# Kernel optimization log

Measured on AMD Instinct MI355X. Metric: run time of the kernel, lower is better.

## Reference

```python
import jax, jax.numpy as jnp
import numpy as np

N_NODES = 50000
N_EDGES = 640000
IN_CH = 128
HIDDEN = 128
HEADS = 4
HEAD_DIM = HIDDEN // HEADS  # 32
NEG_SLOPE = 0.2


def setup_inputs() -> dict:
    key = jax.random.key(0)
    ks = jax.random.split(key, 12)
    x = jax.random.normal(ks[0], (N_NODES, IN_CH), dtype=jnp.float32)
    edge_index = jax.random.randint(ks[1], (2, N_EDGES), 0, N_NODES, dtype=jnp.int64)
    s = 0.1
    W1 = jax.random.normal(ks[2], (IN_CH, HEADS * HEAD_DIM), dtype=jnp.float32) * s
    a_src1 = jax.random.normal(ks[3], (HEADS, HEAD_DIM), dtype=jnp.float32) * s
    a_dst1 = jax.random.normal(ks[4], (HEADS, HEAD_DIM), dtype=jnp.float32) * s
    b1 = jax.random.normal(ks[5], (HEADS * HEAD_DIM,), dtype=jnp.float32) * s
    W2 = jax.random.normal(ks[6], (HIDDEN, HEADS * HEAD_DIM), dtype=jnp.float32) * s
    a_src2 = jax.random.normal(ks[7], (HEADS, HEAD_DIM), dtype=jnp.float32) * s
    a_dst2 = jax.random.normal(ks[8], (HEADS, HEAD_DIM), dtype=jnp.float32) * s
    b2 = jax.random.normal(ks[9], (HEADS * HEAD_DIM,), dtype=jnp.float32) * s
    return {"x": x, "edge_index": edge_index, "W1": W1, "a_src1": a_src1,
            "a_dst1": a_dst1, "b1": b1, "W2": W2, "a_src2": a_src2,
            "a_dst2": a_dst2, "b2": b2}


def _gat_conv(x, src, dst, W, a_src, a_dst, b):
    """PyG GATConv (concat=True, add_self_loops already applied to src/dst)."""
    N = x.shape[0]
    H, C = a_src.shape
    h = (x @ W).reshape(N, H, C)                      # [N, H, C]
    alpha_s = jnp.einsum('nhc,hc->nh', h, a_src)      # [N, H]
    alpha_d = jnp.einsum('nhc,hc->nh', h, a_dst)      # [N, H]
    e = alpha_s[src] + alpha_d[dst]                   # [E, H]
    e = jnp.where(e > 0, e, NEG_SLOPE * e)            # leaky_relu(0.2)
    # segment softmax over destination nodes (every node has a self-loop)
    emax = jax.ops.segment_max(e, dst, num_segments=N)
    ee = jnp.exp(e - emax[dst])
    denom = jax.ops.segment_sum(ee, dst, num_segments=N)
    alpha = ee / (denom[dst] + 1e-16)                 # [E, H]
    out = jax.ops.segment_sum(h[src] * alpha[:, :, None], dst, num_segments=N)
    return out.reshape(N, H * C) + b


def reference(x, edge_index, W1, a_src1, a_dst1, b1, W2, a_src2, a_dst2, b2):
    N = x.shape[0]
    loops = jnp.arange(N, dtype=edge_index.dtype)
    src = jnp.concatenate([edge_index[0], loops])
    dst = jnp.concatenate([edge_index[1], loops])
    h = _gat_conv(x, src, dst, W1, a_src1, a_dst1, b1)
    h = jax.nn.relu(h)  # dropout is identity in eval mode
    out = _gat_conv(h, src, dst, W2, a_src2, a_dst2, b2)
    return out
```

## Files before the change

### kernel.cpp

```cpp
#include <hip/hip_runtime.h>
#include <hip/hip_bf16.h>
#include <hip/hip_fp16.h>

#define N_NODES 50000
#define N_EDGES 640000
#define E_TOT   690000
#define CH      128
#define ROWPAD  50176
#define GEMMB   391
#define EBLK    2048
#define NEB     337
#define NBUCK   196
#define CAP     4608

typedef __attribute__((ext_vector_type(8))) short short8;
typedef __attribute__((ext_vector_type(4))) float float4v;

static __device__ __forceinline__ float bf2f(unsigned short u) {
  return __uint_as_float(((unsigned)u) << 16);
}
static __device__ __forceinline__ unsigned short f2bf(float f) {
  unsigned u = __float_as_uint(f);
  return (unsigned short)((u + 0x7fffu + ((u >> 16) & 1u)) >> 16);
}

static __device__ __forceinline__ void load_edge(const int* __restrict__ ei,
                                                 int e, int i64, int& s, int& d)
{
  if (e >= N_EDGES) { s = d = e - N_EDGES; return; }
  if (i64) { s = ei[2 * (size_t)e]; d = ei[2 * ((size_t)N_EDGES + e)]; }
  else     { s = ei[e];             d = ei[N_EDGES + e]; }
}

static __device__ __forceinline__ short8 load_bf8(const void* __restrict__ X,
                                                  size_t off, int f32)
{
  if (!f32) return *(const short8*)((const unsigned short*)X + off);
  const float4* p = (const float4*)((const float*)X + off);
  float4 u = p[0], v = p[1];
  short8 r;
  r[0] = (short)f2bf(u.x); r[1] = (short)f2bf(u.y);
  r[2] = (short)f2bf(u.z); r[3] = (short)f2bf(u.w);
  r[4] = (short)f2bf(v.x); r[5] = (short)f2bf(v.y);
  r[6] = (short)f2bf(v.z); r[7] = (short)f2bf(v.w);
  return r;
}

__global__ __launch_bounds__(256) void k_prep(
    const void* __restrict__ W1, const void* __restrict__ W2,
    const void* __restrict__ as1, const void* __restrict__ ad1,
    const void* __restrict__ as2, const void* __restrict__ ad2,
    unsigned short* __restrict__ Wt1, unsigned short* __restrict__ Wt2,
    unsigned short* __restrict__ Ba1, unsigned short* __restrict__ Ba2,
    const unsigned short* __restrict__ x16,
    const unsigned int* __restrict__ eiw,
    int* __restrict__ flags, int* __restrict__ gcur)
{
  int b = blockIdx.x, t = threadIdx.x;
  __shared__ int sf, si;
  if (t == 0) { sf = 0; si = 1; }
  __syncthreads();
  int bad = 0;
  for (int i = t; i < 4096; i += 256) {
    float v = bf2f(x16[i]);
    if (!(v == v) || fabsf(v) > 100.f) bad = 1;
  }
  if (bad) atomicOr(&sf, 1);
  if (b == 0 && t < 128 && eiw[2 * t + 1] != 0u) atomicAnd(&si, 0);
  __syncthreads();
  int f32 = sf;
  if (b == 0 && t == 0) { flags[0] = sf; flags[1] = si; }
  if (b == 0 && t < NBUCK) gcur[t] = t * CAP;

  if (b < 8) {
    int g = b * 256 + t;
    int l = g >> 10;
    int rem = g & 1023;
    int k = rem >> 3, n = rem & 7;
    const void* W  = l ? W2 : W1;
    const void* av = (n < 4) ? (l ? as2 : as1) : (l ? ad2 : ad1);
    int h = n & 3;
    float sum = 0.f;
    for (int c = 0; c < 32; c++) {
      float w = f32 ? ((const float*)W)[k * 128 + h * 32 + c]
                    : bf2f(((const unsigned short*)W)[k * 128 + h * 32 + c]);
      float a = f32 ? ((const float*)av)[h * 32 + c]
                    : bf2f(((const unsigned short*)av)[h * 32 + c]);
      sum += w * a;
    }
    unsigned short* Ba = l ? Ba2 : Ba1;
    Ba[n * 128 + k] = f2bf(sum);
    Ba[(8 + (rem >> 7)) * 128 + (rem & 127)] = 0;
  } else {
    int b2 = b - 8;
    int l = b2 >> 7, c = b2 & 127;
    if (t < 128) {
      const void* W = l ? W2 : W1;
      unsigned short* Wt = l ? Wt2 : Wt1;
      Wt[c * 128 + t] = f32 ? f2bf(((const float*)W)[t * 128 + c])
                            : ((const unsigned short*)W)[t * 128 + c];
    }
  }
}

struct SmemG { unsigned short WB[144][136]; };

static __device__ __forceinline__ void gemm_body(
    SmemG& sm, int bx,
    const void* __restrict__ X,
    const unsigned short* __restrict__ Wt_g,
    const unsigned short* __restrict__ Ba_g,
    unsigned short* __restrict__ H, float* __restrict__ AS,
    float* __restrict__ AD, int nrows, int xf32)
{
  int tid = threadIdx.x;
#pragma unroll
  for (int i = 0; i < 8; i++) {
    int j = i * 256 + tid;
    int c = j >> 4, k8 = j & 15;
    *(short8*)&sm.WB[c][k8 * 8] = *(const short8*)(Wt_g + c * 128 + k8 * 8);
  }
  {
    int n = tid >> 4, k8 = tid & 15;
    *(short8*)&sm.WB[128 + n][k8 * 8] = *(const short8*)(Ba_g + n * 128 + k8 * 8);
  }
  __syncthreads();
  int wave = tid >> 6, lane = tid & 63;
  int R0 = (bx * 4 + wave) * 32;
  if (R0 >= nrows) return;
  int m = lane & 15, quad = lane >> 4;
  int rA = R0 + m;        if (rA >= nrows) rA = nrows - 1;
  int rB = R0 + 16 + m;   if (rB >= nrows) rB = nrows - 1;
  size_t aA = (size_t)rA * CH + quad * 8;
  size_t aB = (size_t)rB * CH + quad * 8;
  float4v acc[2][8];
  float4v accA[2];
#pragma unroll
  for (int hf = 0; hf < 2; hf++) {
    accA[hf] = (float4v){0.f, 0.f, 0.f, 0.f};
#pragma unroll
    for (int ct = 0; ct < 8; ct++) acc[hf][ct] = (float4v){0.f, 0.f, 0.f, 0.f};
  }
#pragma unroll
  for (int kb = 0; kb < 4; kb++) {
    short8 a0 = load_bf8(X, aA + kb * 32, xf32);
    short8 a1 = load_bf8(X, aB + kb * 32, xf32);
#pragma unroll
    for (int ct = 0; ct < 8; ct++) {
      short8 bb = *(const short8*)&sm.WB[ct * 16 + m][kb * 32 + quad * 8];
      acc[0][ct] = __builtin_amdgcn_mfma_f32_16x16x32_bf16(a0, bb, acc[0][ct], 0, 0, 0);
      acc[1][ct] = __builtin_amdgcn_mfma_f32_16x16x32_bf16(a1, bb, acc[1][ct], 0, 0, 0);
    }
    short8 bA = *(const short8*)&sm.WB[128 + m][kb * 32 + quad * 8];
    accA[0] = __builtin_amdgcn_mfma_f32_16x16x32_bf16(a0, bA, accA[0], 0, 0, 0);
    accA[1] = __builtin_amdgcn_mfma_f32_16x16x32_bf16(a1, bA, accA[1], 0, 0, 0);
  }
#pragma unroll
  for (int hf = 0; hf < 2; hf++) {
    int rbase = R0 + hf * 16 + quad * 4;
#pragma unroll
    for (int ct = 0; ct < 8; ct++) {
      int col = ct * 16 + m;
#pragma unroll
      for (int r = 0; r < 4; r++)
        H[(size_t)(rbase + r) * CH + col] = __half_as_ushort(__float2half(acc[hf][ct][r]));
    }
    if (m < 4) {
#pragma unroll
      for (int r = 0; r < 4; r++)
        AS[(size_t)(rbase + r) * 4 + m] = accA[hf][r];
    } else if (m < 8) {
#pragma unroll
      for (int r = 0; r < 4; r++)
        AD[(size_t)(rbase + r) * 4 + (m - 4)] = accA[hf][r];
    }
  }
}

__global__ __launch_bounds__(256, 2) void k_gemm(
    const void* __restrict__ X,
    const unsigned short* __restrict__ Wt_g,
    const unsigned short* __restrict__ Ba_g,
    unsigned short* __restrict__ H, float* __restrict__ AS, float* __restrict__ AD,
    int nrows)
{
  __shared__ SmemG sm;
  gemm_body(sm, blockIdx.x, X, Wt_g, Ba_g, H, AS, AD, nrows, 0);
}

__global__ __launch_bounds__(256, 2) void k_gemm_scat(
    const void* __restrict__ X,
    const unsigned short* __restrict__ Wt_g,
    const unsigned short* __restrict__ Ba_g,
    unsigned short* __restrict__ H, float* __restrict__ AS, float* __restrict__ AD,
    int nrows, const int* __restrict__ ei, int* __restrict__ gcur,
    unsigned int* __restrict__ ebuf, const int* __restrict__ flags)
{
  __shared__ SmemG sm;
  __shared__ int hist[NBUCK];
  __shared__ int cur[NBUCK];
  if (blockIdx.x >= GEMMB) {
    int b = blockIdx.x - GEMMB;
    int t = threadIdx.x;
    if (t < NBUCK) hist[t] = 0;
    __syncthreads();
    int i64 = flags[1];
    int base = b * EBLK;
    int sA[8], dA[8];
#pragma unroll
    for (int k = 0; k < 8; k++) {
      int e = base + k * 256 + t;
      sA[k] = -1;
      if (e < E_TOT) {
        load_edge(ei, e, i64, sA[k], dA[k]);
        atomicAdd(&hist[dA[k] >> 8], 1);
      }
    }
    __syncthreads();
    if (t < NBUCK) {
      int c = hist[t];
      cur[t] = c ? atomicAdd(&gcur[t], c) : 0;
    }
    __syncthreads();
#pragma unroll
    for (int k = 0; k < 8; k++) {
      if (sA[k] >= 0) {
        int pos = atomicAdd(&cur[dA[k] >> 8], 1);
        ebuf[pos] = ((unsigned)sA[k] << 8) | (unsigned)(dA[k] & 255);
      }
    }
    return;
  }
  gemm_body(sm, blockIdx.x, X, Wt_g, Ba_g, H, AS, AD, nrows, flags[0]);
}

__global__ __launch_bounds__(256) void k_fine(
    const unsigned int* __restrict__ ebuf, const int* __restrict__ gcur,
    int2* __restrict__ rpdeg, unsigned short* __restrict__ csr)
{
  __shared__ int cnt[256], sh[256], cur[256];
  int q = blockIdx.x, t = threadIdx.x;
  int lo = q * CAP, hi = gcur[q];
  cnt[t] = 0;
  __syncthreads();
  for (int i = lo + t; i < hi; i += 256)
    atomicAdd(&cnt[ebuf[i] & 255u], 1);
  __syncthreads();
  int v = cnt[t];
  sh[t] = v;
  __syncthreads();
  for (int off = 1; off < 256; off <<= 1) {
    int u = (t >= off) ? sh[t - off] : 0;
    __syncthreads();
    sh[t] += u;
    __syncthreads();
  }
  int lp = sh[t] - v;
  int n = (q << 8) + t;
  if (n < N_NODES) rpdeg[n] = make_int2(lo + lp, v);
  cur[t] = lo + lp;
  __syncthreads();
  for (int i = lo + t; i < hi; i += 256) {
    unsigned p = ebuf[i];
    int slot = atomicAdd(&cur[p & 255u], 1);
    csr[slot] = (unsigned short)(p >> 8);
  }
}

__global__ __launch_bounds__(256) void k_agg(
    const int2* __restrict__ rpdeg,
    const unsigned short* __restrict__ csr,
    const __half* __restrict__ H,
    const float* __restrict__ AS, const float* __restrict__ AD,
    const void* __restrict__ b, void* __restrict__ Y,
    const int* __restrict__ flags, int layer)
{
  int tid = threadIdx.x;
  int node = blockIdx.x * 4 + (tid >> 6);
  if (node >= N_NODES) return;
  int lane = tid & 63;
  int h = lane >> 4;
  int c0 = 2 * lane;
  int2 rd = rpdeg[node];
  int start = rd.x, dg = rd.y;
  float adh = AD[(size_t)node * 4 + h];
  const __half2* __restrict__ H2 = (const __half2*)H;
  float accx = 0.f, accy = 0.f, den = 0.f;
  int last = start + dg - 1;
  for (int j = 0; j < dg; j += 16) {
    int sI[16];
#pragma unroll
    for (int u = 0; u < 16; u++) {
      int idx = start + j + u;
      sI[u] = (int)csr[idx <= last ? idx : last];
    }
    float2 vV[16];
#pragma unroll
    for (int u = 0; u < 16; u++)
      vV[u] = __half22float2(H2[sI[u] * 64 + lane]);
    float eV[16];
#pragma unroll
    for (int u = 0; u < 16; u++)
      eV[u] = AS[sI[u] * 4 + h] + adh;
#pragma unroll
    for (int u = 0; u < 16; u++) {
      float x = eV[u] > 0.f ? eV[u] : 0.2f * eV[u];
      float ex = (j + u < dg) ? __expf(x) : 0.f;
      accx += ex * vV[u].x;
      accy += ex * vV[u].y;
      den  += ex;
    }
  }
  float inv = 1.f / (den + 1e-16f);
  int f32 = flags[0];
  float b0 = f32 ? ((const float*)b)[c0]     : bf2f(((const unsigned short*)b)[c0]);
  float b1 = f32 ? ((const float*)b)[c0 + 1] : bf2f(((const unsigned short*)b)[c0 + 1]);
  float r0 = accx * inv + b0;
  float r1 = accy * inv + b1;
  size_t o = (size_t)node * CH + c0;
  if (layer == 1) {
    r0 = r0 > 0.f ? r0 : 0.f;
    r1 = r1 > 0.f ? r1 : 0.f;
    ushort2 w; w.x = f2bf(r0); w.y = f2bf(r1);
    *(ushort2*)((unsigned short*)Y + o) = w;
  } else if (f32) {
    float2 w; w.x = r0; w.y = r1;
    *(float2*)((float*)Y + o) = w;
  } else {
    ushort2 w; w.x = f2bf(r0); w.y = f2bf(r1);
    *(ushort2*)((unsigned short*)Y + o) = w;
  }
}

extern "C" void kernel_launch(void* const* d_in, const int* in_sizes, int n_in,
                              void* d_out, int out_size, void* d_ws, size_t ws_size,
                              hipStream_t stream)
{
  const void* x   = d_in[0];
  const int*  ei  = (const int*)d_in[1];
  const void* W1  = d_in[2];
  const void* as1 = d_in[3];
  const void* ad1 = d_in[4];
  const void* b1  = d_in[5];
  const void* W2  = d_in[6];
  const void* as2 = d_in[7];
  const void* ad2 = d_in[8];
  const void* b2  = d_in[9];

  char* ws = (char*)d_ws;
  unsigned short* H   = (unsigned short*)(ws);
  float*  AS          = (float*)(ws + 12845056);
  float*  AD          = (float*)(ws + 13647872);
  unsigned short* X2  = (unsigned short*)(ws + 14450688);
  int2*   rpdeg       = (int2*)(ws + 27295744);
  unsigned short* csr = (unsigned short*)(ws + 27695744);
  unsigned int* ebuf  = (unsigned int*)(ws + 29502080);
  int*    gcur        = (int*)(ws + 33114752);
  int*    flags       = (int*)(ws + 33115648);
  unsigned short* Wt1 = (unsigned short*)(ws + 33116672);
  unsigned short* Wt2 = (unsigned short*)(ws + 33149440);
  unsigned short* Ba1 = (unsigned short*)(ws + 33182208);
  unsigned short* Ba2 = (unsigned short*)(ws + 33186304);

  const int agg_blocks = (N_NODES + 3) / 4;

  k_prep<<<264, 256, 0, stream>>>(W1, W2, as1, ad1, as2, ad2,
                                  Wt1, Wt2, Ba1, Ba2,
                                  (const unsigned short*)x,
                                  (const unsigned int*)ei, flags, gcur);

  k_gemm_scat<<<GEMMB + NEB, 256, 0, stream>>>(
      x, Wt1, Ba1, H, AS, AD, N_NODES, ei, gcur, ebuf, flags);

  k_fine<<<NBUCK, 256, 0, stream>>>(ebuf, gcur, rpdeg, csr);

  k_agg<<<agg_blocks, 256, 0, stream>>>(rpdeg, csr,
                                        (const __half*)H, AS, AD,
                                        b1, X2, flags, 1);

  k_gemm<<<GEMMB, 256, 0, stream>>>(X2, Wt2, Ba2, H, AS, AD, N_NODES);
  k_agg<<<agg_blocks, 256, 0, stream>>>(rpdeg, csr,
                                        (const __half*)H, AS, AD,
                                        b2, d_out, flags, 2);
}
```

Measured before the change: 212.2 us.

## Fuse layer-1 aggregation with layer-2 GEMM through shared memory

Adds a kernel in which each block aggregates 128 nodes for layer 1 (softmax-weighted gather, bias, ReLU). It writes the bf16 results into shared memory and then runs the layer-2 MFMA projection and attention-logit GEMM on that tile. This removes the global X2 round trip and one kernel launch, and layer 2 now writes to separate H/AS/AD buffers. The trade-off is parallelism: the fused kernel uses only 391 blocks, and each wave walks 32 nodes in sequence. That leaves far fewer waves in flight to hide gather latency than the previous 12500-block aggregation kernel had.

```diff
diff --git a/kernel.cpp b/kernel.cpp
--- a/kernel.cpp
+++ b/kernel.cpp
@@ -105,6 +105,23 @@
 
 struct SmemG { unsigned short WB[144][136]; };
 
+static __device__ __forceinline__ void stage_wb(
+    SmemG& sm, const unsigned short* __restrict__ Wt_g,
+    const unsigned short* __restrict__ Ba_g)
+{
+  int tid = threadIdx.x;
+#pragma unroll
+  for (int i = 0; i < 8; i++) {
+    int j = i * 256 + tid;
+    int c = j >> 4, k8 = j & 15;
+    *(short8*)&sm.WB[c][k8 * 8] = *(const short8*)(Wt_g + c * 128 + k8 * 8);
+  }
+  {
+    int n = tid >> 4, k8 = tid & 15;
+    *(short8*)&sm.WB[128 + n][k8 * 8] = *(const short8*)(Ba_g + n * 128 + k8 * 8);
+  }
+}
+
 static __device__ __forceinline__ void gemm_body(
     SmemG& sm, int bx,
     const void* __restrict__ X,
@@ -114,16 +131,7 @@
     float* __restrict__ AD, int nrows, int xf32)
 {
   int tid = threadIdx.x;
-#pragma unroll
-  for (int i = 0; i < 8; i++) {
-    int j = i * 256 + tid;
-    int c = j >> 4, k8 = j & 15;
-    *(short8*)&sm.WB[c][k8 * 8] = *(const short8*)(Wt_g + c * 128 + k8 * 8);
-  }
-  {
-    int n = tid >> 4, k8 = tid & 15;
-    *(short8*)&sm.WB[128 + n][k8 * 8] = *(const short8*)(Ba_g + n * 128 + k8 * 8);
-  }
+  stage_wb(sm, Wt_g, Ba_g);
   __syncthreads();
   int wave = tid >> 6, lane = tid & 63;
   int R0 = (bx * 4 + wave) * 32;
@@ -175,17 +183,6 @@
         AD[(size_t)(rbase + r) * 4 + (m - 4)] = accA[hf][r];
     }
   }
-}
-
-__global__ __launch_bounds__(256, 2) void k_gemm(
-    const void* __restrict__ X,
-    const unsigned short* __restrict__ Wt_g,
-    const unsigned short* __restrict__ Ba_g,
-    unsigned short* __restrict__ H, float* __restrict__ AS, float* __restrict__ AD,
-    int nrows)
-{
-  __shared__ SmemG sm;
-  gemm_body(sm, blockIdx.x, X, Wt_g, Ba_g, H, AS, AD, nrows, 0);
 }
 
 __global__ __launch_bounds__(256, 2) void k_gemm_scat(
@@ -267,13 +264,139 @@
   }
 }
 
+static __device__ __forceinline__ void agg_node(
+    const unsigned short* __restrict__ csr,
+    const __half2* __restrict__ H2,
+    const float* __restrict__ AS, float adh,
+    int start, int dg, int lane, int h,
+    float& accx, float& accy, float& den)
+{
+  int last = start + dg - 1;
+  for (int j = 0; j < dg; j += 16) {
+    int sI[16];
+#pragma unroll
+    for (int u = 0; u < 16; u++) {
+      int idx = start + j + u;
+      sI[u] = (int)csr[idx <= last ? idx : last];
+    }
+    float2 vV[16];
+#pragma unroll
+    for (int u = 0; u < 16; u++)
+      vV[u] = __half22float2(H2[sI[u] * 64 + lane]);
+    float eV[16];
+#pragma unroll
+    for (int u = 0; u < 16; u++)
+      eV[u] = AS[sI[u] * 4 + h] + adh;
+#pragma unroll
+    for (int u = 0; u < 16; u++) {
+      float x = eV[u] > 0.f ? eV[u] : 0.2f * eV[u];
+      float ex = (j + u < dg) ? __expf(x) : 0.f;
+      accx += ex * vV[u].x;
+      accy += ex * vV[u].y;
+      den  += ex;
+    }
+  }
+}
+
+struct SmemF { unsigned short WB[144][136]; unsigned short X2t[128][136]; };
+
+__global__ __launch_bounds__(256, 2) void k_agg_gemm(
+    const int2* __restrict__ rpdeg,
+    const unsigned short* __restrict__ csr,
+    const __half* __restrict__ H_in,
+    const float* __restrict__ AS_in, const float* __restrict__ AD_in,
+    const void* __restrict__ b1,
+    const unsigned short* __restrict__ Wt_g,
+    const unsigned short* __restrict__ Ba_g,
+    unsigned short* __restrict__ H, float* __restrict__ AS, float* __restrict__ AD,
+    const int* __restrict__ flags)
+{
+  __shared__ SmemF sm;
+  int tid = threadIdx.x;
+  stage_wb(*(SmemG*)&sm, Wt_g, Ba_g);
+
+  int wave = tid >> 6, lane = tid & 63;
+  int h = lane >> 4;
+  int c0 = 2 * lane;
+  int f32 = flags[0];
+  const __half2* __restrict__ H2 = (const __half2*)H_in;
+  float b0 = f32 ? ((const float*)b1)[c0]     : bf2f(((const unsigned short*)b1)[c0]);
+  float bb1 = f32 ? ((const float*)b1)[c0 + 1] : bf2f(((const unsigned short*)b1)[c0 + 1]);
+
+  for (int i = 0; i < 32; i++) {
+    int loc = wave * 32 + i;
+    int node = blockIdx.x * 128 + loc;
+    float r0 = 0.f, r1 = 0.f;
+    if (node < N_NODES) {
+      int2 rd = rpdeg[node];
+      float adh = AD_in[(size_t)node * 4 + h];
+      float accx = 0.f, accy = 0.f, den = 0.f;
+      agg_node(csr, H2, AS_in, adh, rd.x, rd.y, lane, h, accx, accy, den);
+      float inv = 1.f / (den + 1e-16f);
+      r0 = accx * inv + b0;
+      r1 = accy * inv + bb1;
+      r0 = r0 > 0.f ? r0 : 0.f;
+      r1 = r1 > 0.f ? r1 : 0.f;
+    }
+    sm.X2t[loc][c0]     = f2bf(r0);
+    sm.X2t[loc][c0 + 1] = f2bf(r1);
+  }
+  __syncthreads();
+
+  int m = lane & 15, quad = lane >> 4;
+  int R0l = wave * 32;
+  float4v acc[2][8];
+  float4v accA[2];
+#pragma unroll
+  for (int hf = 0; hf < 2; hf++) {
+    accA[hf] = (float4v){0.f, 0.f, 0.f, 0.f};
+#pragma unroll
+    for (int ct = 0; ct < 8; ct++) acc[hf][ct] = (float4v){0.f, 0.f, 0.f, 0.f};
+  }
+#pragma unroll
+  for (int kb = 0; kb < 4; kb++) {
+    short8 a0 = *(const short8*)&sm.X2t[R0l + m][kb * 32 + quad * 8];
+    short8 a1 = *(const short8*)&sm.X2t[R0l + 16 + m][kb * 32 + quad * 8];
+#pragma unroll
+    for (int ct = 0; ct < 8; ct++) {
+      short8 bb = *(const short8*)&sm.WB[ct * 16 + m][kb * 32 + quad * 8];
+      acc[0][ct] = __builtin_amdgcn_mfma_f32_16x16x32_bf16(a0, bb, acc[0][ct], 0, 0, 0);
+      acc[1][ct] = __builtin_amdgcn_mfma_f32_16x16x32_bf16(a1, bb, acc[1][ct], 0, 0, 0);
+    }
+    short8 bA = *(const short8*)&sm.WB[128 + m][kb * 32 + quad * 8];
+    accA[0] = __builtin_amdgcn_mfma_f32_16x16x32_bf16(a0, bA, accA[0], 0, 0, 0);
+    accA[1] = __builtin_amdgcn_mfma_f32_16x16x32_bf16(a1, bA, accA[1], 0, 0, 0);
+  }
+  int Rg = blockIdx.x * 128 + R0l;
+#pragma unroll
+  for (int hf = 0; hf < 2; hf++) {
+    int rbase = Rg + hf * 16 + quad * 4;
+#pragma unroll
+    for (int ct = 0; ct < 8; ct++) {
+      int col = ct * 16 + m;
+#pragma unroll
+      for (int r = 0; r < 4; r++)
+        H[(size_t)(rbase + r) * CH + col] = __half_as_ushort(__float2half(acc[hf][ct][r]));
+    }
+    if (m < 4) {
+#pragma unroll
+      for (int r = 0; r < 4; r++)
+        AS[(size_t)(rbase + r) * 4 + m] = accA[hf][r];
+    } else if (m < 8) {
+#pragma unroll
+      for (int r = 0; r < 4; r++)
+        AD[(size_t)(rbase + r) * 4 + (m - 4)] = accA[hf][r];
+    }
+  }
+}
+
 __global__ __launch_bounds__(256) void k_agg(
     const int2* __restrict__ rpdeg,
     const unsigned short* __restrict__ csr,
     const __half* __restrict__ H,
     const float* __restrict__ AS, const float* __restrict__ AD,
     const void* __restrict__ b, void* __restrict__ Y,
-    const int* __restrict__ flags, int layer)
+    const int* __restrict__ flags)
 {
   int tid = threadIdx.x;
   int node = blockIdx.x * 4 + (tid >> 6);
@@ -282,35 +405,10 @@
   int h = lane >> 4;
   int c0 = 2 * lane;
   int2 rd = rpdeg[node];
-  int start = rd.x, dg = rd.y;
   float adh = AD[(size_t)node * 4 + h];
   const __half2* __restrict__ H2 = (const __half2*)H;
   float accx = 0.f, accy = 0.f, den = 0.f;
-  int last = start + dg - 1;
-  for (int j = 0; j < dg; j += 16) {
-    int sI[16];
-#pragma unroll
-    for (int u = 0; u < 16; u++) {
-      int idx = start + j + u;
-      sI[u] = (int)csr[idx <= last ? idx : last];
-    }
-    float2 vV[16];
-#pragma unroll
-    for (int u = 0; u < 16; u++)
-      vV[u] = __half22float2(H2[sI[u] * 64 + lane]);
-    float eV[16];
-#pragma unroll
-    for (int u = 0; u < 16; u++)
-      eV[u] = AS[sI[u] * 4 + h] + adh;
-#pragma unroll
-    for (int u = 0; u < 16; u++) {
-      float x = eV[u] > 0.f ? eV[u] : 0.2f * eV[u];
-      float ex = (j + u < dg) ? __expf(x) : 0.f;
-      accx += ex * vV[u].x;
-      accy += ex * vV[u].y;
-      den  += ex;
-    }
-  }
+  agg_node(csr, H2, AS, adh, rd.x, rd.y, lane, h, accx, accy, den);
   float inv = 1.f / (den + 1e-16f);
   int f32 = flags[0];
   float b0 = f32 ? ((const float*)b)[c0]     : bf2f(((const unsigned short*)b)[c0]);
@@ -318,12 +416,7 @@
   float r0 = accx * inv + b0;
   float r1 = accy * inv + b1;
   size_t o = (size_t)node * CH + c0;
-  if (layer == 1) {
-    r0 = r0 > 0.f ? r0 : 0.f;
-    r1 = r1 > 0.f ? r1 : 0.f;
-    ushort2 w; w.x = f2bf(r0); w.y = f2bf(r1);
-    *(ushort2*)((unsigned short*)Y + o) = w;
-  } else if (f32) {
+  if (f32) {
     float2 w; w.x = r0; w.y = r1;
     *(float2*)((float*)Y + o) = w;
   } else {
@@ -351,16 +444,18 @@
   unsigned short* H   = (unsigned short*)(ws);
   float*  AS          = (float*)(ws + 12845056);
   float*  AD          = (float*)(ws + 13647872);
-  unsigned short* X2  = (unsigned short*)(ws + 14450688);
-  int2*   rpdeg       = (int2*)(ws + 27295744);
-  unsigned short* csr = (unsigned short*)(ws + 27695744);
-  unsigned int* ebuf  = (unsigned int*)(ws + 29502080);
-  int*    gcur        = (int*)(ws + 33114752);
-  int*    flags       = (int*)(ws + 33115648);
-  unsigned short* Wt1 = (unsigned short*)(ws + 33116672);
-  unsigned short* Wt2 = (unsigned short*)(ws + 33149440);
-  unsigned short* Ba1 = (unsigned short*)(ws + 33182208);
-  unsigned short* Ba2 = (unsigned short*)(ws + 33186304);
+  unsigned short* H2b = (unsigned short*)(ws + 14450688);
+  float*  AS2         = (float*)(ws + 27295744);
+  float*  AD2         = (float*)(ws + 28098560);
+  int2*   rpdeg       = (int2*)(ws + 28901376);
+  unsigned short* csr = (unsigned short*)(ws + 29301376);
+  unsigned int* ebuf  = (unsigned int*)(ws + 31107712);
+  int*    gcur        = (int*)(ws + 34720384);
+  int*    flags       = (int*)(ws + 34721280);
+  unsigned short* Wt1 = (unsigned short*)(ws + 34722304);
+  unsigned short* Wt2 = (unsigned short*)(ws + 34755072);
+  unsigned short* Ba1 = (unsigned short*)(ws + 34787840);
+  unsigned short* Ba2 = (unsigned short*)(ws + 34791936);
 
   const int agg_blocks = (N_NODES + 3) / 4;
 
@@ -374,12 +469,11 @@
 
   k_fine<<<NBUCK, 256, 0, stream>>>(ebuf, gcur, rpdeg, csr);
 
+  k_agg_gemm<<<GEMMB, 256, 0, stream>>>(rpdeg, csr,
+                                        (const __half*)H, AS, AD, b1,
+                                        Wt2, Ba2, H2b, AS2, AD2, flags);
+
   k_agg<<<agg_blocks, 256, 0, stream>>>(rpdeg, csr,
-                                        (const __half*)H, AS, AD,
-                                        b1, X2, flags, 1);
-
-  k_gemm<<<GEMMB, 256, 0, stream>>>(X2, Wt2, Ba2, H, AS, AD, N_NODES);
-  k_agg<<<agg_blocks, 256, 0, stream>>>(rpdeg, csr,
-                                        (const __half*)H, AS, AD,
-                                        b2, d_out, flags, 2);
-}
+                                        (const __half*)H2b, AS2, AD2,
+                                        b2, d_out, flags);
+}
```

Result: slower. 241.6 us (+13.8%).
